# Performance work log

Measured on AMD Instinct MI355X. Metric: run time of the kernel, lower is better.

The kernel has to match this reference:

```python
import jax, jax.numpy as jnp
import numpy as np
from jax import lax

DIM = 192
WS = 8
NH = 6


def setup_inputs() -> dict:
    key = jax.random.key(0)
    ks = jax.random.split(key, 7)
    B, H, W, C = 8, 128, 128, DIM
    s = 1.0 / np.sqrt(C)
    x = jax.random.normal(ks[0], (B, H, W, C), dtype=jnp.float32)
    w_qkv = jax.random.normal(ks[1], (C, 3 * C), dtype=jnp.float32) * s
    b_qkv = jnp.zeros((3 * C,), dtype=jnp.float32)
    # depthwise 3x3 conv kernel in HWIO layout with feature_group_count=C -> (3,3,1,C)
    w_dw = jax.random.normal(ks[2], (3, 3, 1, C), dtype=jnp.float32) * (1.0 / 3.0)
    b_dw = jnp.zeros((C,), dtype=jnp.float32)
    w_proj = jax.random.normal(ks[3], (C, C), dtype=jnp.float32) * s
    b_proj = jnp.zeros((C,), dtype=jnp.float32)
    return {"x": x, "w_qkv": w_qkv, "b_qkv": b_qkv, "w_dw": w_dw,
            "b_dw": b_dw, "w_proj": w_proj, "b_proj": b_proj}


def reference(x, w_qkv, b_qkv, w_dw, b_dw, w_proj, b_proj):
    B, H, W, C = x.shape
    hd = C // NH
    # qkv projection: [B,H,W,3C]
    qkv = x @ w_qkv + b_qkv
    # window partition: (3, B*nWh*nWw*NH, WS*WS, hd)
    qkv = qkv.reshape(B, H // WS, WS, W // WS, WS, 3, NH, hd)
    qkv = qkv.transpose(5, 0, 1, 3, 6, 2, 4, 7).reshape(3, -1, WS * WS, hd)
    q, k, v = qkv[0], qkv[1], qkv[2]
    q = q * (hd ** -0.5)
    attn = jax.nn.softmax(jnp.einsum('wik,wjk->wij', q, k), axis=-1)
    o = jnp.einsum('wij,wjk->wik', attn, v)
    # window reverse -> [B,H,W,C]
    o = o.reshape(B, H // WS, W // WS, NH, WS, WS, hd)
    o = o.transpose(0, 1, 4, 2, 5, 3, 6).reshape(B, H, W, C)
    # proj tail: depthwise 3x3 conv (pad=1) then linear
    o = lax.conv_general_dilated(o, w_dw, window_strides=(1, 1),
                                 padding=[(1, 1), (1, 1)],
                                 dimension_numbers=('NHWC', 'HWIO', 'NHWC'),
                                 feature_group_count=C) + b_dw
    o = o @ w_proj + b_proj
    return o
```

## Files before the change

### kernel.cpp

```cpp
#include <hip/hip_runtime.h>


typedef __attribute__((ext_vector_type(8))) short bf16x8;
typedef __attribute__((ext_vector_type(4))) float f32x4;

__device__ __forceinline__ float bf2f(unsigned short h) {
    return __builtin_bit_cast(float, (unsigned int)h << 16);
}
__device__ __forceinline__ unsigned short f2bf(float f) {
    unsigned int u = __builtin_bit_cast(unsigned int, f);
    u += 0x7fffu + ((u >> 16) & 1u);
    return (unsigned short)(u >> 16);
}
__device__ __forceinline__ bf16x8 ld8(const unsigned short* p) {
    return *(const bf16x8*)p;
}
__device__ __forceinline__ bf16x8 ldf8(const float* p) {
    float4 a = *(const float4*)p;
    float4 b = *(const float4*)(p + 4);
    bf16x8 r;
    r[0] = (short)f2bf(a.x); r[1] = (short)f2bf(a.y);
    r[2] = (short)f2bf(a.z); r[3] = (short)f2bf(a.w);
    r[4] = (short)f2bf(b.x); r[5] = (short)f2bf(b.y);
    r[6] = (short)f2bf(b.z); r[7] = (short)f2bf(b.w);
    return r;
}

__global__ __launch_bounds__(256) void repack_kernel(
    const float* __restrict__ w_qkv, const float* __restrict__ w_proj,
    unsigned short* __restrict__ wq_m, unsigned short* __restrict__ wp_m)
{
    int f = blockIdx.x * 256 + threadIdx.x;
    if (f < 6 * 36 * 64 * 8) {
        int j = f & 7, lane = (f >> 3) & 63, rest = f >> 9;
        int nt = rest % 36, kt = rest / 36;
        wq_m[f] = f2bf(w_qkv[(kt * 32 + (lane >> 4) * 8 + j) * 576 + nt * 16 + (lane & 15)]);
    }
    if (f < 6 * 12 * 64 * 8) {
        int j = f & 7, lane = (f >> 3) & 63, rest = f >> 9;
        int nt = rest % 12, kt = rest / 12;
        wp_m[f] = f2bf(w_proj[(kt * 32 + (lane >> 4) * 8 + j) * 192 + nt * 16 + (lane & 15)]);
    }
}

__global__ __launch_bounds__(256, 2) void qkv_gemm_kernel(
    const float* __restrict__ x, const unsigned short* __restrict__ wq_m,
    const float* __restrict__ b_qkv,
    unsigned short* __restrict__ q_scr, unsigned short* __restrict__ k_scr,
    unsigned short* __restrict__ v_scr)
{
    __shared__ unsigned short vbuf[192 * 72];

    const int tid = threadIdx.x, lane = tid & 63, wave = tid >> 6;
    const int l16 = lane & 15, quad = lane >> 4;
    const int wi = blockIdx.x;
    const int img = wi >> 8, wrem = wi & 255;
    const int y0 = (wrem >> 4) * 8, x0 = (wrem & 15) * 8;

    const float* xrow[4];
#pragma unroll
    for (int mt = 0; mt < 4; ++mt) {
        int token = mt * 16 + l16;
        xrow[mt] = x + ((img * 128 + y0 + (token >> 3)) * 128 + (x0 + (token & 7))) * 192;
    }

    f32x4 acc[9][4];
#pragma unroll
    for (int s = 0; s < 9; ++s)
#pragma unroll
        for (int mt = 0; mt < 4; ++mt) acc[s][mt] = (f32x4){0.f, 0.f, 0.f, 0.f};

    for (int kt = 0; kt < 6; ++kt) {
        bf16x8 af[4];
#pragma unroll
        for (int mt = 0; mt < 4; ++mt) af[mt] = ldf8(xrow[mt] + kt * 32 + quad * 8);
#pragma unroll
        for (int s = 0; s < 9; ++s) {
            bf16x8 bw = ld8(wq_m + (((kt * 36 + wave * 9 + s) * 64 + lane) << 3));
#pragma unroll
            for (int mt = 0; mt < 4; ++mt)
                acc[s][mt] = __builtin_amdgcn_mfma_f32_16x16x32_bf16(af[mt], bw, acc[s][mt], 0, 0, 0);
        }
    }

#pragma unroll
    for (int s = 0; s < 9; ++s) {
        int nt = wave * 9 + s;
        int sec = nt / 12, loc = nt % 12, head = loc >> 1, dh = loc & 1;
        float bias = b_qkv[nt * 16 + l16];
        if (sec == 2) {
            int dim = loc * 16 + l16;
#pragma unroll
            for (int mt = 0; mt < 4; ++mt)
#pragma unroll
                for (int r = 0; r < 4; ++r)
                    vbuf[dim * 72 + mt * 16 + quad * 4 + r] = f2bf(acc[s][mt][r] + bias);
        } else {
            unsigned short* dst = (sec == 0 ? q_scr : k_scr)
                                + ((wi * 6 + head) * 64) * 32 + dh * 16 + l16;
            float scl = (sec == 0) ? 0.17677669529663687f : 1.0f;
#pragma unroll
            for (int mt = 0; mt < 4; ++mt)
#pragma unroll
                for (int r = 0; r < 4; ++r)
                    dst[(mt * 16 + quad * 4 + r) * 32] = f2bf((acc[s][mt][r] + bias) * scl);
        }
    }
    __syncthreads();

#pragma unroll
    for (int k = 0; k < 6; ++k) {
        int idx = k * 256 + tid;
        int oct = idx & 7, dim = idx >> 3;
        bf16x8 t8 = ld8(&vbuf[dim * 72 + oct * 8]);
        *(bf16x8*)&v_scr[(wi * 192 + dim) * 64 + oct * 8] = t8;
    }
}

__global__ __launch_bounds__(64) void attn_kernel(
    const unsigned short* __restrict__ q_scr, const unsigned short* __restrict__ k_scr,
    const unsigned short* __restrict__ v_scr, unsigned short* __restrict__ o_scr)
{
    __shared__ unsigned short Ps[64 * 72];

    const int lane = threadIdx.x, l16 = lane & 15, quad = lane >> 4;
    const int h = blockIdx.x, wi = blockIdx.y;
    const int img = wi >> 8, wrem = wi & 255;
    const int y0 = (wrem >> 4) * 8, x0 = (wrem & 15) * 8;

    const unsigned short* qb = q_scr + ((wi * 6 + h) * 64) * 32;
    const unsigned short* kb = k_scr + ((wi * 6 + h) * 64) * 32;

    bf16x8 aq[4], bk[4];
#pragma unroll
    for (int mt = 0; mt < 4; ++mt) aq[mt] = ld8(qb + (mt * 16 + l16) * 32 + quad * 8);
#pragma unroll
    for (int nt = 0; nt < 4; ++nt) bk[nt] = ld8(kb + (nt * 16 + l16) * 32 + quad * 8);

    f32x4 s[4][4];
#pragma unroll
    for (int mt = 0; mt < 4; ++mt)
#pragma unroll
        for (int nt = 0; nt < 4; ++nt) {
            s[mt][nt] = (f32x4){0.f, 0.f, 0.f, 0.f};
            s[mt][nt] = __builtin_amdgcn_mfma_f32_16x16x32_bf16(aq[mt], bk[nt], s[mt][nt], 0, 0, 0);
        }

#pragma unroll
    for (int mt = 0; mt < 4; ++mt) {
#pragma unroll
        for (int r = 0; r < 4; ++r) {
            float m = fmaxf(fmaxf(s[mt][0][r], s[mt][1][r]), fmaxf(s[mt][2][r], s[mt][3][r]));
            m = fmaxf(m, __shfl_xor(m, 1, 64));
            m = fmaxf(m, __shfl_xor(m, 2, 64));
            m = fmaxf(m, __shfl_xor(m, 4, 64));
            m = fmaxf(m, __shfl_xor(m, 8, 64));
            float pv[4], sum = 0.f;
#pragma unroll
            for (int nt = 0; nt < 4; ++nt) { pv[nt] = __expf(s[mt][nt][r] - m); sum += pv[nt]; }
            sum += __shfl_xor(sum, 1, 64);
            sum += __shfl_xor(sum, 2, 64);
            sum += __shfl_xor(sum, 4, 64);
            sum += __shfl_xor(sum, 8, 64);
            float inv = 1.f / sum;
            int row = mt * 16 + quad * 4 + r;
#pragma unroll
            for (int nt = 0; nt < 4; ++nt)
                Ps[row * 72 + nt * 16 + l16] = f2bf(pv[nt] * inv);
        }
    }
    __syncthreads();

    f32x4 o[4][2];
#pragma unroll
    for (int mt = 0; mt < 4; ++mt)
#pragma unroll
        for (int n2 = 0; n2 < 2; ++n2) o[mt][n2] = (f32x4){0.f, 0.f, 0.f, 0.f};

#pragma unroll
    for (int kt2 = 0; kt2 < 2; ++kt2) {
        bf16x8 bv[2];
#pragma unroll
        for (int n2 = 0; n2 < 2; ++n2)
            bv[n2] = ld8(&v_scr[(wi * 192 + h * 32 + n2 * 16 + l16) * 64 + kt2 * 32 + quad * 8]);
#pragma unroll
        for (int mt = 0; mt < 4; ++mt) {
            bf16x8 ap = ld8(&Ps[(mt * 16 + l16) * 72 + kt2 * 32 + quad * 8]);
#pragma unroll
            for (int n2 = 0; n2 < 2; ++n2)
                o[mt][n2] = __builtin_amdgcn_mfma_f32_16x16x32_bf16(ap, bv[n2], o[mt][n2], 0, 0, 0);
        }
    }

#pragma unroll
    for (int mt = 0; mt < 4; ++mt)
#pragma unroll
        for (int n2 = 0; n2 < 2; ++n2)
#pragma unroll
            for (int r = 0; r < 4; ++r) {
                int token = mt * 16 + quad * 4 + r;
                o_scr[((img * 128 + y0 + (token >> 3)) * 128 + (x0 + (token & 7))) * 192
                      + h * 32 + n2 * 16 + l16] = f2bf(o[mt][n2][r]);
            }
}

__global__ __launch_bounds__(256, 2) void conv_proj_kernel(
    const unsigned short* __restrict__ o_scr,
    const float* __restrict__ w_dw, const float* __restrict__ b_dw,
    const unsigned short* __restrict__ wp_m, const float* __restrict__ b_proj,
    float* __restrict__ out)
{
    __shared__ unsigned short oh[100 * 192];
    __shared__ unsigned short cb[64 * 200];
    __shared__ float wdw_s[9 * 192];
    __shared__ float bdw_s[192];

    const int tid = threadIdx.x, lane = tid & 63, wave = tid >> 6;
    const int l16 = lane & 15, quad = lane >> 4;
    const int img = blockIdx.x >> 8, wrem = blockIdx.x & 255;
    const int y0 = (wrem >> 4) * 8, x0 = (wrem & 15) * 8;

    for (int i = tid; i < 9 * 192; i += 256) wdw_s[i] = w_dw[i];
    if (tid < 192) bdw_s[tid] = b_dw[tid];

    for (int c = tid; c < 2400; c += 256) {
        int pix = c / 24, ck = c % 24;
        int py = y0 - 1 + pix / 10, px = x0 - 1 + pix % 10;
        uint4 v = {0u, 0u, 0u, 0u};
        if (py >= 0 && py < 128 && px >= 0 && px < 128)
            v = *(const uint4*)(o_scr + ((img * 128 + py) * 128 + px) * 192 + ck * 8);
        *(uint4*)(oh + pix * 192 + ck * 8) = v;
    }
    __syncthreads();

#pragma unroll
    for (int k = 0; k < 6; ++k) {
        int idx = k * 256 + tid;
        int c8 = idx % 24, t = idx / 24;
        int r = t >> 3, cc = t & 7;
        float a[8];
#pragma unroll
        for (int i = 0; i < 8; ++i) a[i] = bdw_s[c8 * 8 + i];
#pragma unroll
        for (int dy = 0; dy < 3; ++dy)
#pragma unroll
            for (int dx = 0; dx < 3; ++dx) {
                bf16x8 hv = ld8(&oh[((r + dy) * 10 + (cc + dx)) * 192 + c8 * 8]);
                const float* wp = &wdw_s[(dy * 3 + dx) * 192 + c8 * 8];
#pragma unroll
                for (int i = 0; i < 8; ++i)
                    a[i] += bf2f((unsigned short)hv[i]) * wp[i];
            }
        bf16x8 rv;
#pragma unroll
        for (int i = 0; i < 8; ++i) rv[i] = (short)f2bf(a[i]);
        *(bf16x8*)&cb[t * 200 + c8 * 8] = rv;
    }
    __syncthreads();

    f32x4 po[3][4];
#pragma unroll
    for (int n = 0; n < 3; ++n)
#pragma unroll
        for (int mt = 0; mt < 4; ++mt) po[n][mt] = (f32x4){0.f, 0.f, 0.f, 0.f};

    for (int kt = 0; kt < 6; ++kt) {
        bf16x8 af[4];
#pragma unroll
        for (int mt = 0; mt < 4; ++mt) af[mt] = ld8(cb + (mt * 16 + l16) * 200 + kt * 32 + quad * 8);
#pragma unroll
        for (int ntl = 0; ntl < 3; ++ntl) {
            bf16x8 bw = ld8(wp_m + (((kt * 12 + wave * 3 + ntl) * 64 + lane) << 3));
#pragma unroll
            for (int mt = 0; mt < 4; ++mt)
                po[ntl][mt] = __builtin_amdgcn_mfma_f32_16x16x32_bf16(af[mt], bw, po[ntl][mt], 0, 0, 0);
        }
    }

#pragma unroll
    for (int ntl = 0; ntl < 3; ++ntl) {
        int col = (wave * 3 + ntl) * 16 + l16;
        float bias = b_proj[col];
#pragma unroll
        for (int mt = 0; mt < 4; ++mt)
#pragma unroll
            for (int r = 0; r < 4; ++r) {
                int t = mt * 16 + quad * 4 + r;
                out[((img * 128 + y0 + (t >> 3)) * 128 + (x0 + (t & 7))) * 192 + col]
                    = po[ntl][mt][r] + bias;
            }
    }
}

__global__ __launch_bounds__(256, 2) void qkv_attn_kernel(
    const float* __restrict__ x, const unsigned short* __restrict__ wq_m,
    const float* __restrict__ b_qkv, unsigned short* __restrict__ o_scr)
{
    __shared__ unsigned short qs[64 * 104];
    __shared__ unsigned short ks[64 * 104];
    __shared__ unsigned short vT[96 * 72];
    __shared__ unsigned short Ps[64 * 72];

    const int tid = threadIdx.x, lane = tid & 63, wave = tid >> 6;
    const int l16 = lane & 15, quad = lane >> 4;
    const int img = blockIdx.x >> 8, wrem = blockIdx.x & 255;
    const int y0 = (wrem >> 4) * 8, x0 = (wrem & 15) * 8;

    const float* xrow[4];
#pragma unroll
    for (int mt = 0; mt < 4; ++mt) {
        int token = mt * 16 + l16;
        xrow[mt] = x + ((img * 128 + y0 + (token >> 3)) * 128 + (x0 + (token & 7))) * 192;
    }
    const int cnt = (wave < 2) ? 5 : 4;
    const int start = (wave < 2) ? wave * 5 : 10 + (wave - 2) * 4;

    for (int p = 0; p < 2; ++p) {
        int nt_g[5], sec[5], tl[5];
#pragma unroll
        for (int s = 0; s < 5; ++s) {
            int ti = start + s, sc = ti / 6, t = ti - sc * 6;
            sec[s] = sc; tl[s] = t; nt_g[s] = sc * 12 + p * 6 + t;
        }
        f32x4 acc[5][4];
#pragma unroll
        for (int s = 0; s < 5; ++s)
#pragma unroll
            for (int mt = 0; mt < 4; ++mt) acc[s][mt] = (f32x4){0.f, 0.f, 0.f, 0.f};

        for (int kt = 0; kt < 6; ++kt) {
            bf16x8 af[4];
#pragma unroll
            for (int mt = 0; mt < 4; ++mt) af[mt] = ldf8(xrow[mt] + kt * 32 + quad * 8);
#pragma unroll
            for (int s = 0; s < 5; ++s)
                if (s < cnt) {
                    bf16x8 bw = ld8(wq_m + (((kt * 36 + nt_g[s]) * 64 + lane) << 3));
#pragma unroll
                    for (int mt = 0; mt < 4; ++mt)
                        acc[s][mt] = __builtin_amdgcn_mfma_f32_16x16x32_bf16(af[mt], bw, acc[s][mt], 0, 0, 0);
                }
        }
#pragma unroll
        for (int s = 0; s < 5; ++s)
            if (s < cnt) {
                float bias = b_qkv[nt_g[s] * 16 + l16];
#pragma unroll
                for (int mt = 0; mt < 4; ++mt)
#pragma unroll
                    for (int r = 0; r < 4; ++r) {
                        int token = mt * 16 + quad * 4 + r;
                        float v = acc[s][mt][r] + bias;
                        if (sec[s] == 0)      qs[token * 104 + tl[s] * 16 + l16] = f2bf(v * 0.17677669529663687f);
                        else if (sec[s] == 1) ks[token * 104 + tl[s] * 16 + l16] = f2bf(v);
                        else                  vT[(tl[s] * 16 + l16) * 72 + token] = f2bf(v);
                    }
            }
        __syncthreads();

        for (int i = 0; i < 3; ++i) {
            bf16x8 aq = ld8(qs + (wave * 16 + l16) * 104 + i * 32 + quad * 8);
            f32x4 sc4[4];
#pragma unroll
            for (int nt = 0; nt < 4; ++nt) {
                sc4[nt] = (f32x4){0.f, 0.f, 0.f, 0.f};
                bf16x8 bk = ld8(ks + (nt * 16 + l16) * 104 + i * 32 + quad * 8);
                sc4[nt] = __builtin_amdgcn_mfma_f32_16x16x32_bf16(aq, bk, sc4[nt], 0, 0, 0);
            }
            float linv[4];
#pragma unroll
            for (int r = 0; r < 4; ++r) {
                float m = fmaxf(fmaxf(sc4[0][r], sc4[1][r]), fmaxf(sc4[2][r], sc4[3][r]));
                m = fmaxf(m, __shfl_xor(m, 1, 64));
                m = fmaxf(m, __shfl_xor(m, 2, 64));
                m = fmaxf(m, __shfl_xor(m, 4, 64));
                m = fmaxf(m, __shfl_xor(m, 8, 64));
                float pv[4], sum = 0.f;
#pragma unroll
                for (int nt = 0; nt < 4; ++nt) { pv[nt] = __expf(sc4[nt][r] - m); sum += pv[nt]; }
                sum += __shfl_xor(sum, 1, 64);
                sum += __shfl_xor(sum, 2, 64);
                sum += __shfl_xor(sum, 4, 64);
                sum += __shfl_xor(sum, 8, 64);
                linv[r] = 1.f / sum;
                int row = wave * 16 + quad * 4 + r;
#pragma unroll
                for (int nt = 0; nt < 4; ++nt) Ps[row * 72 + nt * 16 + l16] = f2bf(pv[nt]);
            }
            __syncthreads();
            f32x4 o4[2];
            o4[0] = (f32x4){0.f, 0.f, 0.f, 0.f};
            o4[1] = (f32x4){0.f, 0.f, 0.f, 0.f};
#pragma unroll
            for (int kt2 = 0; kt2 < 2; ++kt2) {
                bf16x8 ap = ld8(Ps + (wave * 16 + l16) * 72 + kt2 * 32 + quad * 8);
#pragma unroll
                for (int nt = 0; nt < 2; ++nt) {
                    bf16x8 bv = ld8(vT + (i * 32 + nt * 16 + l16) * 72 + kt2 * 32 + quad * 8);
                    o4[nt] = __builtin_amdgcn_mfma_f32_16x16x32_bf16(ap, bv, o4[nt], 0, 0, 0);
                }
            }
            int h = p * 3 + i;
#pragma unroll
            for (int nt = 0; nt < 2; ++nt)
#pragma unroll
                for (int r = 0; r < 4; ++r) {
                    int token = wave * 16 + quad * 4 + r;
                    o_scr[((img * 128 + y0 + (token >> 3)) * 128 + (x0 + (token & 7))) * 192
                          + h * 32 + nt * 16 + l16] = f2bf(o4[nt][r] * linv[r]);
                }
            __syncthreads();
        }
        __syncthreads();
    }
}

extern "C" void kernel_launch(void* const* d_in, const int* in_sizes, int n_in,
                              void* d_out, int out_size, void* d_ws, size_t ws_size,
                              hipStream_t stream)
{
    const float* x      = (const float*)d_in[0];
    const float* w_qkv  = (const float*)d_in[1];
    const float* b_qkv  = (const float*)d_in[2];
    const float* w_dw   = (const float*)d_in[3];
    const float* b_dw   = (const float*)d_in[4];
    const float* w_proj = (const float*)d_in[5];
    const float* b_proj = (const float*)d_in[6];
    float* out = (float*)d_out;

    unsigned short* wq_m  = (unsigned short*)d_ws;
    unsigned short* wp_m  = wq_m + 110592;
    unsigned short* o_scr = wq_m + 147456;
    unsigned short* q_scr = wq_m + 25313280;
    unsigned short* k_scr = wq_m + 50479104;
    unsigned short* v_scr = wq_m + 75644928;

    bool fast = ws_size >= (size_t)100810752 * 2;

    repack_kernel<<<dim3(432), dim3(256), 0, stream>>>(w_qkv, w_proj, wq_m, wp_m);
    if (fast) {
        qkv_gemm_kernel<<<dim3(2048), dim3(256), 0, stream>>>(x, wq_m, b_qkv, q_scr, k_scr, v_scr);
        attn_kernel<<<dim3(6, 2048), dim3(64), 0, stream>>>(q_scr, k_scr, v_scr, o_scr);
    } else {
        qkv_attn_kernel<<<dim3(2048), dim3(256), 0, stream>>>(x, wq_m, b_qkv, o_scr);
    }
    conv_proj_kernel<<<dim3(2048), dim3(256), 0, stream>>>(o_scr, w_dw, b_dw, wp_m, b_proj, out);
}
```

Measured before the change: 354.7 us.

## Fuse QKV projection and window attention into one kernel with one wave per head

```diff
diff --git a/kernel.cpp b/kernel.cpp
--- a/kernel.cpp
+++ b/kernel.cpp
@@ -43,40 +43,50 @@
     }
 }
 
-__global__ __launch_bounds__(256, 2) void qkv_gemm_kernel(
+__global__ __launch_bounds__(384) void qkv_attn_fused(
     const float* __restrict__ x, const unsigned short* __restrict__ wq_m,
-    const float* __restrict__ b_qkv,
-    unsigned short* __restrict__ q_scr, unsigned short* __restrict__ k_scr,
-    unsigned short* __restrict__ v_scr)
+    const float* __restrict__ b_qkv, unsigned short* __restrict__ o_scr)
 {
-    __shared__ unsigned short vbuf[192 * 72];
-
-    const int tid = threadIdx.x, lane = tid & 63, wave = tid >> 6;
+    __shared__ unsigned short smem[12800 + 6 * 7424];
+
+    const int tid = threadIdx.x, lane = tid & 63, h = tid >> 6;
     const int l16 = lane & 15, quad = lane >> 4;
     const int wi = blockIdx.x;
     const int img = wi >> 8, wrem = wi & 255;
     const int y0 = (wrem >> 4) * 8, x0 = (wrem & 15) * 8;
 
-    const float* xrow[4];
-#pragma unroll
-    for (int mt = 0; mt < 4; ++mt) {
-        int token = mt * 16 + l16;
-        xrow[mt] = x + ((img * 128 + y0 + (token >> 3)) * 128 + (x0 + (token & 7))) * 192;
-    }
-
-    f32x4 acc[9][4];
-#pragma unroll
-    for (int s = 0; s < 9; ++s)
+    {
+        const int token = tid / 6, seg = tid % 6;
+        const float* sp = x + ((img * 128 + y0 + (token >> 3)) * 128
+                               + (x0 + (token & 7))) * 192 + seg * 32;
+        unsigned short* dp = smem + token * 200 + seg * 32;
+#pragma unroll
+        for (int i = 0; i < 4; ++i)
+            *(bf16x8*)(dp + i * 8) = ldf8(sp + i * 8);
+    }
+    __syncthreads();
+
+    unsigned short* qs = smem + 12800 + h * 7424;
+    unsigned short* ks = qs + 2560;
+    unsigned short* vT = qs + 5120;
+    unsigned short* Ps = qs;
+
+    const int ntb[6] = {2 * h, 2 * h + 1, 12 + 2 * h, 13 + 2 * h, 24 + 2 * h, 25 + 2 * h};
+
+    f32x4 acc[6][4];
+#pragma unroll
+    for (int s = 0; s < 6; ++s)
 #pragma unroll
         for (int mt = 0; mt < 4; ++mt) acc[s][mt] = (f32x4){0.f, 0.f, 0.f, 0.f};
 
     for (int kt = 0; kt < 6; ++kt) {
         bf16x8 af[4];
 #pragma unroll
-        for (int mt = 0; mt < 4; ++mt) af[mt] = ldf8(xrow[mt] + kt * 32 + quad * 8);
-#pragma unroll
-        for (int s = 0; s < 9; ++s) {
-            bf16x8 bw = ld8(wq_m + (((kt * 36 + wave * 9 + s) * 64 + lane) << 3));
+        for (int mt = 0; mt < 4; ++mt)
+            af[mt] = ld8(smem + (mt * 16 + l16) * 200 + kt * 32 + quad * 8);
+#pragma unroll
+        for (int s = 0; s < 6; ++s) {
+            bf16x8 bw = ld8(wq_m + (((kt * 36 + ntb[s]) * 64 + lane) << 3));
 #pragma unroll
             for (int mt = 0; mt < 4; ++mt)
                 acc[s][mt] = __builtin_amdgcn_mfma_f32_16x16x32_bf16(af[mt], bw, acc[s][mt], 0, 0, 0);
@@ -84,92 +94,70 @@
     }
 
 #pragma unroll
-    for (int s = 0; s < 9; ++s) {
-        int nt = wave * 9 + s;
-        int sec = nt / 12, loc = nt % 12, head = loc >> 1, dh = loc & 1;
-        float bias = b_qkv[nt * 16 + l16];
-        if (sec == 2) {
-            int dim = loc * 16 + l16;
+    for (int s = 0; s < 6; ++s) {
+        const float bias = b_qkv[ntb[s] * 16 + l16];
+        if (s < 2) {
 #pragma unroll
             for (int mt = 0; mt < 4; ++mt)
 #pragma unroll
                 for (int r = 0; r < 4; ++r)
-                    vbuf[dim * 72 + mt * 16 + quad * 4 + r] = f2bf(acc[s][mt][r] + bias);
+                    qs[(mt * 16 + quad * 4 + r) * 40 + s * 16 + l16] =
+                        f2bf((acc[s][mt][r] + bias) * 0.17677669529663687f);
+        } else if (s < 4) {
+#pragma unroll
+            for (int mt = 0; mt < 4; ++mt)
+#pragma unroll
+                for (int r = 0; r < 4; ++r)
+                    ks[(mt * 16 + quad * 4 + r) * 40 + (s - 2) * 16 + l16] =
+                        f2bf(acc[s][mt][r] + bias);
         } else {
-            unsigned short* dst = (sec == 0 ? q_scr : k_scr)
-                                + ((wi * 6 + head) * 64) * 32 + dh * 16 + l16;
-            float scl = (sec == 0) ? 0.17677669529663687f : 1.0f;
 #pragma unroll
             for (int mt = 0; mt < 4; ++mt)
 #pragma unroll
                 for (int r = 0; r < 4; ++r)
-                    dst[(mt * 16 + quad * 4 + r) * 32] = f2bf((acc[s][mt][r] + bias) * scl);
-        }
-    }
-    __syncthreads();
-
-#pragma unroll
-    for (int k = 0; k < 6; ++k) {
-        int idx = k * 256 + tid;
-        int oct = idx & 7, dim = idx >> 3;
-        bf16x8 t8 = ld8(&vbuf[dim * 72 + oct * 8]);
-        *(bf16x8*)&v_scr[(wi * 192 + dim) * 64 + oct * 8] = t8;
-    }
-}
-
-__global__ __launch_bounds__(64) void attn_kernel(
-    const unsigned short* __restrict__ q_scr, const unsigned short* __restrict__ k_scr,
-    const unsigned short* __restrict__ v_scr, unsigned short* __restrict__ o_scr)
-{
-    __shared__ unsigned short Ps[64 * 72];
-
-    const int lane = threadIdx.x, l16 = lane & 15, quad = lane >> 4;
-    const int h = blockIdx.x, wi = blockIdx.y;
-    const int img = wi >> 8, wrem = wi & 255;
-    const int y0 = (wrem >> 4) * 8, x0 = (wrem & 15) * 8;
-
-    const unsigned short* qb = q_scr + ((wi * 6 + h) * 64) * 32;
-    const unsigned short* kb = k_scr + ((wi * 6 + h) * 64) * 32;
+                    vT[((s - 4) * 16 + l16) * 72 + mt * 16 + quad * 4 + r] =
+                        f2bf(acc[s][mt][r] + bias);
+        }
+    }
 
     bf16x8 aq[4], bk[4];
 #pragma unroll
-    for (int mt = 0; mt < 4; ++mt) aq[mt] = ld8(qb + (mt * 16 + l16) * 32 + quad * 8);
-#pragma unroll
-    for (int nt = 0; nt < 4; ++nt) bk[nt] = ld8(kb + (nt * 16 + l16) * 32 + quad * 8);
-
-    f32x4 s[4][4];
+    for (int mt = 0; mt < 4; ++mt) aq[mt] = ld8(qs + (mt * 16 + l16) * 40 + quad * 8);
+#pragma unroll
+    for (int nt = 0; nt < 4; ++nt) bk[nt] = ld8(ks + (nt * 16 + l16) * 40 + quad * 8);
+
+    f32x4 s4[4][4];
 #pragma unroll
     for (int mt = 0; mt < 4; ++mt)
 #pragma unroll
         for (int nt = 0; nt < 4; ++nt) {
-            s[mt][nt] = (f32x4){0.f, 0.f, 0.f, 0.f};
-            s[mt][nt] = __builtin_amdgcn_mfma_f32_16x16x32_bf16(aq[mt], bk[nt], s[mt][nt], 0, 0, 0);
+            s4[mt][nt] = (f32x4){0.f, 0.f, 0.f, 0.f};
+            s4[mt][nt] = __builtin_amdgcn_mfma_f32_16x16x32_bf16(aq[mt], bk[nt], s4[mt][nt], 0, 0, 0);
         }
 
 #pragma unroll
     for (int mt = 0; mt < 4; ++mt) {
 #pragma unroll
         for (int r = 0; r < 4; ++r) {
-            float m = fmaxf(fmaxf(s[mt][0][r], s[mt][1][r]), fmaxf(s[mt][2][r], s[mt][3][r]));
+            float m = fmaxf(fmaxf(s4[mt][0][r], s4[mt][1][r]), fmaxf(s4[mt][2][r], s4[mt][3][r]));
             m = fmaxf(m, __shfl_xor(m, 1, 64));
             m = fmaxf(m, __shfl_xor(m, 2, 64));
             m = fmaxf(m, __shfl_xor(m, 4, 64));
             m = fmaxf(m, __shfl_xor(m, 8, 64));
             float pv[4], sum = 0.f;
 #pragma unroll
-            for (int nt = 0; nt < 4; ++nt) { pv[nt] = __expf(s[mt][nt][r] - m); sum += pv[nt]; }
+            for (int nt = 0; nt < 4; ++nt) { pv[nt] = __expf(s4[mt][nt][r] - m); sum += pv[nt]; }
             sum += __shfl_xor(sum, 1, 64);
             sum += __shfl_xor(sum, 2, 64);
             sum += __shfl_xor(sum, 4, 64);
             sum += __shfl_xor(sum, 8, 64);
-            float inv = 1.f / sum;
-            int row = mt * 16 + quad * 4 + r;
+            const float inv = 1.f / sum;
+            const int row = mt * 16 + quad * 4 + r;
 #pragma unroll
             for (int nt = 0; nt < 4; ++nt)
                 Ps[row * 72 + nt * 16 + l16] = f2bf(pv[nt] * inv);
         }
     }
-    __syncthreads();
 
     f32x4 o[4][2];
 #pragma unroll
@@ -182,10 +170,10 @@
         bf16x8 bv[2];
 #pragma unroll
         for (int n2 = 0; n2 < 2; ++n2)
-            bv[n2] = ld8(&v_scr[(wi * 192 + h * 32 + n2 * 16 + l16) * 64 + kt2 * 32 + quad * 8]);
+            bv[n2] = ld8(vT + (n2 * 16 + l16) * 72 + kt2 * 32 + quad * 8);
 #pragma unroll
         for (int mt = 0; mt < 4; ++mt) {
-            bf16x8 ap = ld8(&Ps[(mt * 16 + l16) * 72 + kt2 * 32 + quad * 8]);
+            bf16x8 ap = ld8(Ps + (mt * 16 + l16) * 72 + kt2 * 32 + quad * 8);
 #pragma unroll
             for (int n2 = 0; n2 < 2; ++n2)
                 o[mt][n2] = __builtin_amdgcn_mfma_f32_16x16x32_bf16(ap, bv[n2], o[mt][n2], 0, 0, 0);
@@ -198,7 +186,7 @@
         for (int n2 = 0; n2 < 2; ++n2)
 #pragma unroll
             for (int r = 0; r < 4; ++r) {
-                int token = mt * 16 + quad * 4 + r;
+                const int token = mt * 16 + quad * 4 + r;
                 o_scr[((img * 128 + y0 + (token >> 3)) * 128 + (x0 + (token & 7))) * 192
                       + h * 32 + n2 * 16 + l16] = f2bf(o[mt][n2][r]);
             }
@@ -289,129 +277,6 @@
                 out[((img * 128 + y0 + (t >> 3)) * 128 + (x0 + (t & 7))) * 192 + col]
                     = po[ntl][mt][r] + bias;
             }
-    }
-}
-
-__global__ __launch_bounds__(256, 2) void qkv_attn_kernel(
-    const float* __restrict__ x, const unsigned short* __restrict__ wq_m,
-    const float* __restrict__ b_qkv, unsigned short* __restrict__ o_scr)
-{
-    __shared__ unsigned short qs[64 * 104];
-    __shared__ unsigned short ks[64 * 104];
-    __shared__ unsigned short vT[96 * 72];
-    __shared__ unsigned short Ps[64 * 72];
-
-    const int tid = threadIdx.x, lane = tid & 63, wave = tid >> 6;
-    const int l16 = lane & 15, quad = lane >> 4;
-    const int img = blockIdx.x >> 8, wrem = blockIdx.x & 255;
-    const int y0 = (wrem >> 4) * 8, x0 = (wrem & 15) * 8;
-
-    const float* xrow[4];
-#pragma unroll
-    for (int mt = 0; mt < 4; ++mt) {
-        int token = mt * 16 + l16;
-        xrow[mt] = x + ((img * 128 + y0 + (token >> 3)) * 128 + (x0 + (token & 7))) * 192;
-    }
-    const int cnt = (wave < 2) ? 5 : 4;
-    const int start = (wave < 2) ? wave * 5 : 10 + (wave - 2) * 4;
-
-    for (int p = 0; p < 2; ++p) {
-        int nt_g[5], sec[5], tl[5];
-#pragma unroll
-        for (int s = 0; s < 5; ++s) {
-            int ti = start + s, sc = ti / 6, t = ti - sc * 6;
-            sec[s] = sc; tl[s] = t; nt_g[s] = sc * 12 + p * 6 + t;
-        }
-        f32x4 acc[5][4];
-#pragma unroll
-        for (int s = 0; s < 5; ++s)
-#pragma unroll
-            for (int mt = 0; mt < 4; ++mt) acc[s][mt] = (f32x4){0.f, 0.f, 0.f, 0.f};
-
-        for (int kt = 0; kt < 6; ++kt) {
-            bf16x8 af[4];
-#pragma unroll
-            for (int mt = 0; mt < 4; ++mt) af[mt] = ldf8(xrow[mt] + kt * 32 + quad * 8);
-#pragma unroll
-            for (int s = 0; s < 5; ++s)
-                if (s < cnt) {
-                    bf16x8 bw = ld8(wq_m + (((kt * 36 + nt_g[s]) * 64 + lane) << 3));
-#pragma unroll
-                    for (int mt = 0; mt < 4; ++mt)
-                        acc[s][mt] = __builtin_amdgcn_mfma_f32_16x16x32_bf16(af[mt], bw, acc[s][mt], 0, 0, 0);
-                }
-        }
-#pragma unroll
-        for (int s = 0; s < 5; ++s)
-            if (s < cnt) {
-                float bias = b_qkv[nt_g[s] * 16 + l16];
-#pragma unroll
-                for (int mt = 0; mt < 4; ++mt)
-#pragma unroll
-                    for (int r = 0; r < 4; ++r) {
-                        int token = mt * 16 + quad * 4 + r;
-                        float v = acc[s][mt][r] + bias;
-                        if (sec[s] == 0)      qs[token * 104 + tl[s] * 16 + l16] = f2bf(v * 0.17677669529663687f);
-                        else if (sec[s] == 1) ks[token * 104 + tl[s] * 16 + l16] = f2bf(v);
-                        else                  vT[(tl[s] * 16 + l16) * 72 + token] = f2bf(v);
-                    }
-            }
-        __syncthreads();
-
-        for (int i = 0; i < 3; ++i) {
-            bf16x8 aq = ld8(qs + (wave * 16 + l16) * 104 + i * 32 + quad * 8);
-            f32x4 sc4[4];
-#pragma unroll
-            for (int nt = 0; nt < 4; ++nt) {
-                sc4[nt] = (f32x4){0.f, 0.f, 0.f, 0.f};
-                bf16x8 bk = ld8(ks + (nt * 16 + l16) * 104 + i * 32 + quad * 8);
-                sc4[nt] = __builtin_amdgcn_mfma_f32_16x16x32_bf16(aq, bk, sc4[nt], 0, 0, 0);
-            }
-            float linv[4];
-#pragma unroll
-            for (int r = 0; r < 4; ++r) {
-                float m = fmaxf(fmaxf(sc4[0][r], sc4[1][r]), fmaxf(sc4[2][r], sc4[3][r]));
-                m = fmaxf(m, __shfl_xor(m, 1, 64));
-                m = fmaxf(m, __shfl_xor(m, 2, 64));
-                m = fmaxf(m, __shfl_xor(m, 4, 64));
-                m = fmaxf(m, __shfl_xor(m, 8, 64));
-                float pv[4], sum = 0.f;
-#pragma unroll
-                for (int nt = 0; nt < 4; ++nt) { pv[nt] = __expf(sc4[nt][r] - m); sum += pv[nt]; }
-                sum += __shfl_xor(sum, 1, 64);
-                sum += __shfl_xor(sum, 2, 64);
-                sum += __shfl_xor(sum, 4, 64);
-                sum += __shfl_xor(sum, 8, 64);
-                linv[r] = 1.f / sum;
-                int row = wave * 16 + quad * 4 + r;
-#pragma unroll
-                for (int nt = 0; nt < 4; ++nt) Ps[row * 72 + nt * 16 + l16] = f2bf(pv[nt]);
-            }
-            __syncthreads();
-            f32x4 o4[2];
-            o4[0] = (f32x4){0.f, 0.f, 0.f, 0.f};
-            o4[1] = (f32x4){0.f, 0.f, 0.f, 0.f};
-#pragma unroll
-            for (int kt2 = 0; kt2 < 2; ++kt2) {
-                bf16x8 ap = ld8(Ps + (wave * 16 + l16) * 72 + kt2 * 32 + quad * 8);
-#pragma unroll
-                for (int nt = 0; nt < 2; ++nt) {
-                    bf16x8 bv = ld8(vT + (i * 32 + nt * 16 + l16) * 72 + kt2 * 32 + quad * 8);
-                    o4[nt] = __builtin_amdgcn_mfma_f32_16x16x32_bf16(ap, bv, o4[nt], 0, 0, 0);
-                }
-            }
-            int h = p * 3 + i;
-#pragma unroll
-            for (int nt = 0; nt < 2; ++nt)
-#pragma unroll
-                for (int r = 0; r < 4; ++r) {
-                    int token = wave * 16 + quad * 4 + r;
-                    o_scr[((img * 128 + y0 + (token >> 3)) * 128 + (x0 + (token & 7))) * 192
-                          + h * 32 + nt * 16 + l16] = f2bf(o4[nt][r] * linv[r]);
-                }
-            __syncthreads();
-        }
-        __syncthreads();
     }
 }
 
@@ -431,18 +296,8 @@
     unsigned short* wq_m  = (unsigned short*)d_ws;
     unsigned short* wp_m  = wq_m + 110592;
     unsigned short* o_scr = wq_m + 147456;
-    unsigned short* q_scr = wq_m + 25313280;
-    unsigned short* k_scr = wq_m + 50479104;
-    unsigned short* v_scr = wq_m + 75644928;
-
-    bool fast = ws_size >= (size_t)100810752 * 2;
 
     repack_kernel<<<dim3(432), dim3(256), 0, stream>>>(w_qkv, w_proj, wq_m, wp_m);
-    if (fast) {
-        qkv_gemm_kernel<<<dim3(2048), dim3(256), 0, stream>>>(x, wq_m, b_qkv, q_scr, k_scr, v_scr);
-        attn_kernel<<<dim3(6, 2048), dim3(64), 0, stream>>>(q_scr, k_scr, v_scr, o_scr);
-    } else {
-        qkv_attn_kernel<<<dim3(2048), dim3(256), 0, stream>>>(x, wq_m, b_qkv, o_scr);
-    }
+    qkv_attn_fused<<<dim3(2048), dim3(384), 0, stream>>>(x, wq_m, b_qkv, o_scr);
     conv_proj_kernel<<<dim3(2048), dim3(256), 0, stream>>>(o_scr, w_dw, b_dw, wp_m, b_proj, out);
 }
```

Measured after the change: 313.4 us. 1.13x faster.
